# Kernel tuning notes

Measured on AMD Instinct MI355X. Metric: run time of the kernel, lower is better.

Reference implementation:

```python
import jax, jax.numpy as jnp
import numpy as np

NUM_NODES_FEAT = 400   # per-graph node count == input feature dim (fMRI ROIs)
F1 = 256
F2 = 256
NUM_GRAPHS = 256
N_TOTAL = NUM_GRAPHS * NUM_NODES_FEAT  # 102400 nodes
E_TOTAL = 4096000                      # ~40 avg degree


def setup_inputs() -> dict:
    key = jax.random.key(0)
    ks = jax.random.split(key, 8)
    x = jax.random.normal(ks[0], (N_TOTAL, NUM_NODES_FEAT), dtype=jnp.float32)
    edge_index = jax.random.randint(ks[1], (2, E_TOTAL), 0, N_TOTAL, dtype=jnp.int64)
    # PyG-style block-diagonal batch vector: 400 nodes per graph
    batch = jnp.repeat(jnp.arange(NUM_GRAPHS, dtype=jnp.int64), NUM_NODES_FEAT)
    # learned params (xavier-ish scale)
    def xavier(k, shape):
        fan_in, fan_out = shape[0], shape[1]
        s = jnp.sqrt(6.0 / (fan_in + fan_out))
        return jax.random.uniform(k, shape, jnp.float32, -s, s)
    W1 = xavier(ks[2], (NUM_NODES_FEAT, F1))
    b1 = jax.random.uniform(ks[3], (F1,), jnp.float32)
    W2 = xavier(ks[4], (F1, F2))
    b2 = jax.random.uniform(ks[5], (F2,), jnp.float32)
    Wm = xavier(ks[6], (2 * F2, 2))   # meanmax readout -> 2*f2 input
    bm = jax.random.uniform(ks[7], (2,), jnp.float32)
    return {"x": x, "edge_index": edge_index, "batch": batch,
            "num_graphs": NUM_GRAPHS,
            "W1": W1, "b1": b1, "W2": W2, "b2": b2, "Wm": Wm, "bm": bm}


def _gcn_conv(x, W, b, src, dst, deg_inv_sqrt, n):
    # PyG GCNConv: linear transform, then deg^{-1/2}-normalized scatter-add
    h = x @ W                                   # [N, f_out]
    norm = deg_inv_sqrt[src] * deg_inv_sqrt[dst]  # [E+N]
    msgs = h[src] * norm[:, None]               # gather + scale
    out = jax.ops.segment_sum(msgs, dst, num_segments=n)
    return out + b


def reference(x, edge_index, batch, num_graphs, W1, b1, W2, b2, Wm, bm):
    n = x.shape[0]
    loops = jnp.arange(n, dtype=edge_index.dtype)
    src = jnp.concatenate([edge_index[0], loops])  # add self-loops (PyG default)
    dst = jnp.concatenate([edge_index[1], loops])
    deg = jax.ops.segment_sum(jnp.ones_like(dst, dtype=x.dtype), dst, num_segments=n)
    deg_inv_sqrt = jnp.where(deg > 0, jax.lax.rsqrt(deg), 0.0)

    h = _gcn_conv(x, W1, b1, src, dst, deg_inv_sqrt, n)
    h = jax.nn.relu(h)
    # F.dropout(training=False) -> identity in eval mode
    h = _gcn_conv(h, W2, b2, src, dst, deg_inv_sqrt, n)

    # meanmax graph readout over batch segments
    g_sum = jax.ops.segment_sum(h, batch, num_segments=num_graphs)
    cnt = jax.ops.segment_sum(jnp.ones((n,), h.dtype), batch, num_segments=num_graphs)
    g_mean = g_sum / jnp.maximum(cnt, 1.0)[:, None]
    g_max = jax.ops.segment_max(h, batch, num_segments=num_graphs)
    g = jnp.concatenate([g_mean, g_max], axis=-1)  # [G, 2*f2]
    return g @ Wm + bm                             # [G, 2]
```

## Files before the change

### kernel.cpp

```cpp
#include <hip/hip_runtime.h>
#include <hip/hip_bf16.h>

#define N_NODES 102400
#define FEAT    400
#define F1      256
#define E_EDGES 4096000
#define NUM_G   256
#define NPG     400
#define NSLICE  8
#define NODES_PER_SLICE (NPG / NSLICE)

#define NBIN    400
#define BINCAP  12288
#define EPB     4096
#define BIN_BLOCKS (E_EDGES / EPB)
#define CVT1_BLOCKS 416
#define CVT2_BLOCKS 256
#define CVT_BLOCKS  (CVT1_BLOCKS + CVT2_BLOCKS)

typedef __attribute__((ext_vector_type(8))) short bfrag;
typedef __attribute__((ext_vector_type(4))) float ffrag;
typedef __attribute__((ext_vector_type(4))) short s4;

__device__ inline short f2b(float f) {
    __hip_bfloat16 h = __float2bfloat16(f);
    return *reinterpret_cast<short*>(&h);
}

#define ACC(uu) { auto vl = __builtin_amdgcn_cvt_pk_f32_fp8(uu, false); \
                  auto vh = __builtin_amdgcn_cvt_pk_f32_fp8(uu, true);  \
                  a0 += vl[0]; a1 += vl[1]; a2 += vh[0]; a3 += vh[1]; }

__global__ __launch_bounds__(256) void k_binA(const int* __restrict__ ei,
                                              int* __restrict__ binfill,
                                              int2* __restrict__ binbuf,
                                              const float* __restrict__ W1,
                                              const float* __restrict__ W2,
                                              short* __restrict__ Wt1,
                                              short* __restrict__ Wt2) {
    const int t = threadIdx.x;
    if (blockIdx.x < BIN_BLOCKS) {
        __shared__ int h[NBIN], base[NBIN], cur[NBIN];
        const int e0 = blockIdx.x * EPB;
        for (int b = t; b < NBIN; b += 256) h[b] = 0;
        __syncthreads();
#pragma unroll 4
        for (int k = 0; k < 16; ++k) {
            int d = ei[E_EDGES + e0 + k * 256 + t];
            atomicAdd(&h[d >> 8], 1);
        }
        __syncthreads();
        for (int b = t; b < NBIN; b += 256) {
            base[b] = atomicAdd(&binfill[b], h[b]);
            cur[b]  = 0;
        }
        __syncthreads();
#pragma unroll 4
        for (int k = 0; k < 16; ++k) {
            int e = e0 + k * 256 + t;
            int s = ei[e];
            int d = ei[E_EDGES + e];
            int bin = d >> 8;
            int idx = base[bin] + atomicAdd(&cur[bin], 1);
            if (idx < BINCAP) binbuf[(size_t)bin * BINCAP + idx] = make_int2(s, d);
        }
    } else {
        int cb = blockIdx.x - BIN_BLOCKS;
        if (cb < CVT1_BLOCKS) {
            int idx = cb * 256 + t;
            int n = idx / 416, k = idx - n * 416;
            float v = (k < 400) ? W1[(size_t)k * 256 + n] : 0.f;
            Wt1[idx] = f2b(v);
        } else {
            int idx = (cb - CVT1_BLOCKS) * 256 + t;
            int n = idx >> 8, k = idx & 255;
            Wt2[idx] = f2b(W2[(size_t)k * 256 + n]);
        }
    }
}

__global__ __launch_bounds__(512) void k_binscan(const int* __restrict__ binfill,
                                                 int* __restrict__ binbase) {
    __shared__ int s[512];
    int t = threadIdx.x;
    int v = (t < NBIN) ? binfill[t] : 0;
    s[t] = v;
    __syncthreads();
    for (int off = 1; off < 512; off <<= 1) {
        int u = (t >= off) ? s[t - off] : 0;
        __syncthreads();
        s[t] += u;
        __syncthreads();
    }
    if (t < NBIN) binbase[t] = s[t] - v;
}

__global__ __launch_bounds__(256) void k_bcnt(const int* __restrict__ binfill,
                                              const int* __restrict__ binbase,
                                              const int2* __restrict__ binbuf,
                                              int* __restrict__ row_start,
                                              float* __restrict__ dis) {
    __shared__ int h[256], sc[256];
    const int b = blockIdx.x, t = threadIdx.x;
    h[t] = 0;
    __syncthreads();
    int n = binfill[b]; if (n > BINCAP) n = BINCAP;
    const int2* p = binbuf + (size_t)b * BINCAP;
    for (int i = t; i < n; i += 256) atomicAdd(&h[p[i].y & 255], 1);
    __syncthreads();
    int deg = h[t];
    sc[t] = deg;
    __syncthreads();
    for (int off = 1; off < 256; off <<= 1) {
        int u = (t >= off) ? sc[t - off] : 0;
        __syncthreads();
        sc[t] += u;
        __syncthreads();
    }
    int node = b * 256 + t;
    row_start[node] = binbase[b] + sc[t] - deg;
    dis[node] = rsqrtf((float)(deg + 1));
    if (b == NBIN - 1 && t == 255) row_start[N_NODES] = binbase[b] + sc[t];
}

template<bool AF32>
__device__ void mm_body(int bm, int bn,
                        const void* __restrict__ Ap,
                        const short* __restrict__ Wt,
                        const float* __restrict__ dis,
                        int Kreal, int Kpad,
                        unsigned char* __restrict__ Cp) {
    __shared__ short As[128][40];
    __shared__ short Bs[128][40];
    const int t    = threadIdx.x;
    const int lane = t & 63;
    const int w    = t >> 6;
    const int wm   = w >> 1, wn = w & 1;
    const int m0   = bm * 128;
    const int n0   = bn * 128;
    const int sr   = t >> 1;
    const int sh   = (t & 1) * 16;

    ffrag acc[4][4];
#pragma unroll
    for (int i = 0; i < 4; ++i)
#pragma unroll
        for (int j = 0; j < 4; ++j) {
            ffrag z = {0.f, 0.f, 0.f, 0.f};
            acc[i][j] = z;
        }

    const int rl = lane & 15;
    const int kc = (lane >> 4) * 8;

    for (int k0 = 0; k0 < Kpad; k0 += 32) {
        short av[16], bv[16];
        if constexpr (AF32) {
            const float* A = (const float*)Ap;
            const float* arow = A + (size_t)(m0 + sr) * Kreal + k0 + sh;
#pragma unroll
            for (int c = 0; c < 4; ++c) {
                float4 v;
                if (k0 + sh + c * 4 < Kreal) v = *(const float4*)(arow + c * 4);
                else                         v = make_float4(0.f, 0.f, 0.f, 0.f);
                av[c * 4 + 0] = f2b(v.x);
                av[c * 4 + 1] = f2b(v.y);
                av[c * 4 + 2] = f2b(v.z);
                av[c * 4 + 3] = f2b(v.w);
            }
        } else {
            const short* A = (const short*)Ap;
            const short* arow = A + (size_t)(m0 + sr) * Kpad + k0 + sh;
            *(bfrag*)&av[0] = *(const bfrag*)arow;
            *(bfrag*)&av[8] = *(const bfrag*)(arow + 8);
        }
        const short* brow = Wt + (size_t)(n0 + sr) * Kpad + k0 + sh;
        *(bfrag*)&bv[0] = *(const bfrag*)brow;
        *(bfrag*)&bv[8] = *(const bfrag*)(brow + 8);

        __syncthreads();
        *(bfrag*)&As[sr][sh]     = *(bfrag*)&av[0];
        *(bfrag*)&As[sr][sh + 8] = *(bfrag*)&av[8];
        *(bfrag*)&Bs[sr][sh]     = *(bfrag*)&bv[0];
        *(bfrag*)&Bs[sr][sh + 8] = *(bfrag*)&bv[8];
        __syncthreads();

        bfrag a[4], b[4];
#pragma unroll
        for (int i = 0; i < 4; ++i) a[i] = *(const bfrag*)&As[wm * 64 + i * 16 + rl][kc];
#pragma unroll
        for (int j = 0; j < 4; ++j) b[j] = *(const bfrag*)&Bs[wn * 64 + j * 16 + rl][kc];
#pragma unroll
        for (int i = 0; i < 4; ++i)
#pragma unroll
            for (int j = 0; j < 4; ++j)
                acc[i][j] = __builtin_amdgcn_mfma_f32_16x16x32_bf16(a[i], b[j], acc[i][j], 0, 0, 0);
    }

    const int rh = lane >> 4;
    float scale[4][4];
#pragma unroll
    for (int i = 0; i < 4; ++i)
#pragma unroll
        for (int q = 0; q < 4; ++q)
            scale[i][q] = dis[m0 + wm * 64 + i * 16 + rh * 4 + q];

#pragma unroll
    for (int i = 0; i < 4; ++i)
#pragma unroll
        for (int j = 0; j < 4; ++j) {
            int col  = n0 + wn * 64 + j * 16 + rl;
            int rowb = m0 + wm * 64 + i * 16 + rh * 4;
#pragma unroll
            for (int q = 0; q < 4; ++q) {
                float v = acc[i][j][q] * scale[i][q];
                int p = __builtin_amdgcn_cvt_pk_fp8_f32(v, 0.f, 0, false);
                Cp[(size_t)(rowb + q) * 256 + col] = (unsigned char)(p & 0xff);
            }
        }
}

__global__ __launch_bounds__(256) void k_fillmm(const int* __restrict__ binfill,
                                                const int2* __restrict__ binbuf,
                                                const int* __restrict__ row_start,
                                                int* __restrict__ csr,
                                                const float* __restrict__ x,
                                                const short* __restrict__ Wt1,
                                                const float* __restrict__ dis,
                                                unsigned char* __restrict__ P8) {
    if (blockIdx.x < NBIN) {
        __shared__ int rs[256], cur[256];
        const int b = blockIdx.x, t = threadIdx.x;
        rs[t]  = row_start[b * 256 + t];
        cur[t] = 0;
        __syncthreads();
        int n = binfill[b]; if (n > BINCAP) n = BINCAP;
        const int2* p = binbuf + (size_t)b * BINCAP;
        for (int i = t; i < n; i += 256) {
            int2 e = p[i];
            int dl = e.y & 255;
            int pos = atomicAdd(&cur[dl], 1);
            csr[rs[dl] + pos] = e.x;
        }
    } else {
        int bx = blockIdx.x - NBIN;
        mm_body<true>(bx >> 1, bx & 1, (const void*)x, Wt1, dis, 400, 416, P8);
    }
}

__global__ __launch_bounds__(256) void k_mm2(const short* __restrict__ Pb,
                                             const short* __restrict__ Wt2,
                                             const float* __restrict__ dis,
                                             unsigned char* __restrict__ P8) {
    mm_body<false>(blockIdx.x, blockIdx.y, (const void*)Pb, Wt2, dis, 256, 256, P8);
}

__global__ __launch_bounds__(256) void k_agg8(const unsigned int* __restrict__ h8,
                                              const float* __restrict__ dis,
                                              const int* __restrict__ row_start,
                                              const int* __restrict__ csr,
                                              const float* __restrict__ bias,
                                              short* __restrict__ out) {
    const int w = threadIdx.x >> 6;
    const int t = threadIdx.x & 63;
    const int i = blockIdx.x * 4 + w;
    float di = dis[i];
    unsigned int u = h8[(size_t)i * 64 + t];
    auto lo = __builtin_amdgcn_cvt_pk_f32_fp8(u, false);
    auto hi = __builtin_amdgcn_cvt_pk_f32_fp8(u, true);
    float a0 = lo[0], a1 = lo[1], a2 = hi[0], a3 = hi[1];

    const int beg = row_start[i], end = row_start[i + 1];
    const int* row = csr + beg;
    const int n = end - beg;
    int j = 0;
    for (; j + 8 <= n; j += 8) {
        unsigned int uu[8];
#pragma unroll
        for (int k = 0; k < 8; ++k) uu[k] = h8[(size_t)row[j + k] * 64 + t];
#pragma unroll
        for (int k = 0; k < 8; ++k) ACC(uu[k])
    }
    for (; j + 4 <= n; j += 4) {
        unsigned int uu[4];
#pragma unroll
        for (int k = 0; k < 4; ++k) uu[k] = h8[(size_t)row[j + k] * 64 + t];
#pragma unroll
        for (int k = 0; k < 4; ++k) ACC(uu[k])
    }
    for (; j < n; ++j) {
        unsigned int uv = h8[(size_t)row[j] * 64 + t];
        ACC(uv)
    }
    float4 bb = *(const float4*)(bias + t * 4);
    s4 o;
    o[0] = f2b(fmaxf(fmaf(di, a0, bb.x), 0.f));
    o[1] = f2b(fmaxf(fmaf(di, a1, bb.y), 0.f));
    o[2] = f2b(fmaxf(fmaf(di, a2, bb.z), 0.f));
    o[3] = f2b(fmaxf(fmaf(di, a3, bb.w), 0.f));
    *(s4*)(out + (size_t)i * 256 + t * 4) = o;
}

__global__ __launch_bounds__(256) void k_agg2f(const unsigned int* __restrict__ h8,
                                               const float* __restrict__ dis,
                                               const int* __restrict__ row_start,
                                               const int* __restrict__ csr,
                                               const float* __restrict__ bias,
                                               float* __restrict__ partial) {
    const int g     = blockIdx.x;
    const int slice = blockIdx.y;
    const int t     = threadIdx.x;
    const int w     = t >> 6;
    const int lane  = t & 63;

    float4 bb = *(const float4*)(bias + lane * 4);
    float sm[4] = {0.f, 0.f, 0.f, 0.f};
    float mx[4] = {-3.402823466e38f, -3.402823466e38f, -3.402823466e38f, -3.402823466e38f};

    const int r0 = slice * NODES_PER_SLICE;
    for (int r = r0 + w; r < r0 + NODES_PER_SLICE; r += 4) {
        int i = g * NPG + r;
        float di = dis[i];
        unsigned int u = h8[(size_t)i * 64 + lane];
        auto lo = __builtin_amdgcn_cvt_pk_f32_fp8(u, false);
        auto hi = __builtin_amdgcn_cvt_pk_f32_fp8(u, true);
        float a0 = lo[0], a1 = lo[1], a2 = hi[0], a3 = hi[1];

        const int beg = row_start[i], end = row_start[i + 1];
        const int* row = csr + beg;
        const int n = end - beg;
        int j = 0;
        for (; j + 8 <= n; j += 8) {
            unsigned int uu[8];
#pragma unroll
            for (int k = 0; k < 8; ++k) uu[k] = h8[(size_t)row[j + k] * 64 + lane];
#pragma unroll
            for (int k = 0; k < 8; ++k) ACC(uu[k])
        }
        for (; j + 4 <= n; j += 4) {
            unsigned int uu[4];
#pragma unroll
            for (int k = 0; k < 4; ++k) uu[k] = h8[(size_t)row[j + k] * 64 + lane];
#pragma unroll
            for (int k = 0; k < 4; ++k) ACC(uu[k])
        }
        for (; j < n; ++j) {
            unsigned int uv = h8[(size_t)row[j] * 64 + lane];
            ACC(uv)
        }
        float h0 = fmaf(di, a0, bb.x);
        float h1 = fmaf(di, a1, bb.y);
        float h2 = fmaf(di, a2, bb.z);
        float h3 = fmaf(di, a3, bb.w);
        sm[0] += h0; sm[1] += h1; sm[2] += h2; sm[3] += h3;
        mx[0] = fmaxf(mx[0], h0); mx[1] = fmaxf(mx[1], h1);
        mx[2] = fmaxf(mx[2], h2); mx[3] = fmaxf(mx[3], h3);
    }

    __shared__ float ls[4][256];
    __shared__ float lm[4][256];
#pragma unroll
    for (int k = 0; k < 4; ++k) {
        ls[w][lane * 4 + k] = sm[k];
        lm[w][lane * 4 + k] = mx[k];
    }
    __syncthreads();
    if (w == 0) {
        float* base = partial + ((size_t)g * NSLICE + slice) * 512;
#pragma unroll
        for (int k = 0; k < 4; ++k) {
            int f = lane * 4 + k;
            base[f]       = ls[0][f] + ls[1][f] + ls[2][f] + ls[3][f];
            base[256 + f] = fmaxf(fmaxf(lm[0][f], lm[1][f]), fmaxf(lm[2][f], lm[3][f]));
        }
    }
}

__global__ __launch_bounds__(256) void k_final(const float* __restrict__ partial,
                                               const float* __restrict__ Wm,
                                               const float* __restrict__ bm,
                                               float* __restrict__ out) {
    int g = blockIdx.x, t = threadIdx.x;
    const float* pg = partial + (size_t)g * NSLICE * 512;
    float sum = 0.f, mxv = -3.402823466e38f;
#pragma unroll
    for (int s = 0; s < NSLICE; ++s) {
        sum += pg[s * 512 + t];
        mxv = fmaxf(mxv, pg[s * 512 + 256 + t]);
    }
    float mean = sum * (1.0f / NPG);
    float p0 = mean * Wm[t * 2 + 0] + mxv * Wm[(256 + t) * 2 + 0];
    float p1 = mean * Wm[t * 2 + 1] + mxv * Wm[(256 + t) * 2 + 1];
    __shared__ float2 red[256];
    red[t] = make_float2(p0, p1);
    __syncthreads();
    for (int s2 = 128; s2 > 0; s2 >>= 1) {
        if (t < s2) {
            red[t].x += red[t + s2].x;
            red[t].y += red[t + s2].y;
        }
        __syncthreads();
    }
    if (t == 0) {
        out[g * 2 + 0] = red[0].x + bm[0];
        out[g * 2 + 1] = red[0].y + bm[1];
    }
}

extern "C" void kernel_launch(void* const* d_in, const int* in_sizes, int n_in,
                              void* d_out, int out_size, void* d_ws, size_t ws_size,
                              hipStream_t stream) {
    const float* x  = (const float*)d_in[0];
    const int*   ei = (const int*)d_in[1];
    const float* W1 = (const float*)d_in[4];
    const float* b1 = (const float*)d_in[5];
    const float* W2 = (const float*)d_in[6];
    const float* b2 = (const float*)d_in[7];
    const float* Wm = (const float*)d_in[8];
    const float* bm = (const float*)d_in[9];
    float* out = (float*)d_out;

    char* ws = (char*)d_ws;
    size_t off = 0;
    auto alloc = [&](size_t bytes) {
        void* p = ws + off;
        off = (off + bytes + 255) & ~(size_t)255;
        return p;
    };
    int*   binfill   = (int*)alloc((size_t)NBIN * 4);
    int*   binbase   = (int*)alloc((size_t)NBIN * 4);
    int2*  binbuf    = (int2*)alloc((size_t)NBIN * BINCAP * 8);
    int*   row_start = (int*)alloc((size_t)(N_NODES + 1) * 4);
    float* dis       = (float*)alloc((size_t)N_NODES * 4);
    int*   csr       = (int*)alloc((size_t)E_EDGES * 4);
    short* Wt1       = (short*)alloc((size_t)256 * 416 * 2);
    short* Wt2       = (short*)alloc((size_t)256 * 256 * 2);
    unsigned char* P8 = (unsigned char*)alloc((size_t)N_NODES * F1);
    short* Pb        = (short*)alloc((size_t)N_NODES * F1 * 2);
    float* partialb  = (float*)alloc((size_t)NUM_G * NSLICE * 512 * 4);

    hipMemsetAsync(binfill, 0, (size_t)NBIN * 4, stream);
    k_binA<<<BIN_BLOCKS + CVT_BLOCKS, 256, 0, stream>>>(ei, binfill, binbuf,
                                                        W1, W2, Wt1, Wt2);
    k_binscan<<<1, 512, 0, stream>>>(binfill, binbase);
    k_bcnt<<<NBIN, 256, 0, stream>>>(binfill, binbase, binbuf, row_start, dis);
    k_fillmm<<<NBIN + 1600, 256, 0, stream>>>(binfill, binbuf, row_start, csr,
                                              x, Wt1, dis, P8);
    k_agg8<<<N_NODES / 4, 256, 0, stream>>>((const unsigned int*)P8, dis, row_start,
                                            csr, b1, Pb);
    k_mm2<<<dim3(800, 2), 256, 0, stream>>>(Pb, Wt2, dis, P8);
    k_agg2f<<<dim3(NUM_G, NSLICE), 256, 0, stream>>>((const unsigned int*)P8, dis,
                                                     row_start, csr, b2, partialb);
    k_final<<<NUM_G, 256, 0, stream>>>(partialb, Wm, bm, out);
}
```

Before: 548.6 us.

## Pack binned edges into 32-bit words, fold bin scan into count kernel, unroll gathers

Binned edges are stored as a single 32-bit word (24-bit source index plus 8-bit local destination) instead of an int2, halving binbuf write and read traffic in the binning, counting and CSR-fill kernels. The separate single-block prefix-scan kernel is removed; each k_bcnt block instead reduces the fill counts of all preceding bins to get its own base, saving a launch at the cost of redundant reads. The gather loops in both aggregation kernels are unrolled from 8 to 16 loads to keep more memory requests in flight, which raises register pressure. The packing assumes node indices fit in 24 bits, which holds for 102400 nodes.

New measurement: 552.0 us. About the same (+0.6%).

```diff
diff --git a/kernel.cpp b/kernel.cpp
--- a/kernel.cpp
+++ b/kernel.cpp
@@ -33,7 +33,7 @@
 
 __global__ __launch_bounds__(256) void k_binA(const int* __restrict__ ei,
                                               int* __restrict__ binfill,
-                                              int2* __restrict__ binbuf,
+                                              unsigned int* __restrict__ binbuf,
                                               const float* __restrict__ W1,
                                               const float* __restrict__ W2,
                                               short* __restrict__ Wt1,
@@ -58,11 +58,12 @@
 #pragma unroll 4
         for (int k = 0; k < 16; ++k) {
             int e = e0 + k * 256 + t;
-            int s = ei[e];
+            unsigned int s = (unsigned int)ei[e];
             int d = ei[E_EDGES + e];
             int bin = d >> 8;
             int idx = base[bin] + atomicAdd(&cur[bin], 1);
-            if (idx < BINCAP) binbuf[(size_t)bin * BINCAP + idx] = make_int2(s, d);
+            if (idx < BINCAP)
+                binbuf[(size_t)bin * BINCAP + idx] = s | ((unsigned int)(d & 255) << 24);
         }
     } else {
         int cb = blockIdx.x - BIN_BLOCKS;
@@ -79,34 +80,31 @@
     }
 }
 
-__global__ __launch_bounds__(512) void k_binscan(const int* __restrict__ binfill,
-                                                 int* __restrict__ binbase) {
-    __shared__ int s[512];
-    int t = threadIdx.x;
-    int v = (t < NBIN) ? binfill[t] : 0;
-    s[t] = v;
-    __syncthreads();
-    for (int off = 1; off < 512; off <<= 1) {
-        int u = (t >= off) ? s[t - off] : 0;
-        __syncthreads();
-        s[t] += u;
-        __syncthreads();
-    }
-    if (t < NBIN) binbase[t] = s[t] - v;
-}
-
 __global__ __launch_bounds__(256) void k_bcnt(const int* __restrict__ binfill,
-                                              const int* __restrict__ binbase,
-                                              const int2* __restrict__ binbuf,
+                                              const unsigned int* __restrict__ binbuf,
                                               int* __restrict__ row_start,
                                               float* __restrict__ dis) {
+    __shared__ int red[256];
     __shared__ int h[256], sc[256];
     const int b = blockIdx.x, t = threadIdx.x;
+
+    int v = 0;
+    if (t < b) v += binfill[t];
+    if (256 + t < b) v += binfill[256 + t];
+    red[t] = v;
+    __syncthreads();
+    for (int s = 128; s > 0; s >>= 1) {
+        if (t < s) red[t] += red[t + s];
+        __syncthreads();
+    }
+    const int binbase = red[0];
+    __syncthreads();
+
     h[t] = 0;
     __syncthreads();
     int n = binfill[b]; if (n > BINCAP) n = BINCAP;
-    const int2* p = binbuf + (size_t)b * BINCAP;
-    for (int i = t; i < n; i += 256) atomicAdd(&h[p[i].y & 255], 1);
+    const unsigned int* p = binbuf + (size_t)b * BINCAP;
+    for (int i = t; i < n; i += 256) atomicAdd(&h[p[i] >> 24], 1);
     __syncthreads();
     int deg = h[t];
     sc[t] = deg;
@@ -118,9 +116,9 @@
         __syncthreads();
     }
     int node = b * 256 + t;
-    row_start[node] = binbase[b] + sc[t] - deg;
+    row_start[node] = binbase + sc[t] - deg;
     dis[node] = rsqrtf((float)(deg + 1));
-    if (b == NBIN - 1 && t == 255) row_start[N_NODES] = binbase[b] + sc[t];
+    if (b == NBIN - 1 && t == 255) row_start[N_NODES] = binbase + sc[t];
 }
 
 template<bool AF32>
@@ -221,7 +219,7 @@
 }
 
 __global__ __launch_bounds__(256) void k_fillmm(const int* __restrict__ binfill,
-                                                const int2* __restrict__ binbuf,
+                                                const unsigned int* __restrict__ binbuf,
                                                 const int* __restrict__ row_start,
                                                 int* __restrict__ csr,
                                                 const float* __restrict__ x,
@@ -235,12 +233,12 @@
         cur[t] = 0;
         __syncthreads();
         int n = binfill[b]; if (n > BINCAP) n = BINCAP;
-        const int2* p = binbuf + (size_t)b * BINCAP;
+        const unsigned int* p = binbuf + (size_t)b * BINCAP;
         for (int i = t; i < n; i += 256) {
-            int2 e = p[i];
-            int dl = e.y & 255;
+            unsigned int e = p[i];
+            int dl = e >> 24;
             int pos = atomicAdd(&cur[dl], 1);
-            csr[rs[dl] + pos] = e.x;
+            csr[rs[dl] + pos] = (int)(e & 0x00FFFFFFu);
         }
     } else {
         int bx = blockIdx.x - NBIN;
@@ -274,12 +272,12 @@
     const int* row = csr + beg;
     const int n = end - beg;
     int j = 0;
-    for (; j + 8 <= n; j += 8) {
-        unsigned int uu[8];
-#pragma unroll
-        for (int k = 0; k < 8; ++k) uu[k] = h8[(size_t)row[j + k] * 64 + t];
-#pragma unroll
-        for (int k = 0; k < 8; ++k) ACC(uu[k])
+    for (; j + 16 <= n; j += 16) {
+        unsigned int uu[16];
+#pragma unroll
+        for (int k = 0; k < 16; ++k) uu[k] = h8[(size_t)row[j + k] * 64 + t];
+#pragma unroll
+        for (int k = 0; k < 16; ++k) ACC(uu[k])
     }
     for (; j + 4 <= n; j += 4) {
         unsigned int uu[4];
@@ -330,12 +328,12 @@
         const int* row = csr + beg;
         const int n = end - beg;
         int j = 0;
-        for (; j + 8 <= n; j += 8) {
-            unsigned int uu[8];
-#pragma unroll
-            for (int k = 0; k < 8; ++k) uu[k] = h8[(size_t)row[j + k] * 64 + lane];
-#pragma unroll
-            for (int k = 0; k < 8; ++k) ACC(uu[k])
+        for (; j + 16 <= n; j += 16) {
+            unsigned int uu[16];
+#pragma unroll
+            for (int k = 0; k < 16; ++k) uu[k] = h8[(size_t)row[j + k] * 64 + lane];
+#pragma unroll
+            for (int k = 0; k < 16; ++k) ACC(uu[k])
         }
         for (; j + 4 <= n; j += 4) {
             unsigned int uu[4];
@@ -427,23 +425,21 @@
         off = (off + bytes + 255) & ~(size_t)255;
         return p;
     };
-    int*   binfill   = (int*)alloc((size_t)NBIN * 4);
-    int*   binbase   = (int*)alloc((size_t)NBIN * 4);
-    int2*  binbuf    = (int2*)alloc((size_t)NBIN * BINCAP * 8);
-    int*   row_start = (int*)alloc((size_t)(N_NODES + 1) * 4);
-    float* dis       = (float*)alloc((size_t)N_NODES * 4);
-    int*   csr       = (int*)alloc((size_t)E_EDGES * 4);
-    short* Wt1       = (short*)alloc((size_t)256 * 416 * 2);
-    short* Wt2       = (short*)alloc((size_t)256 * 256 * 2);
-    unsigned char* P8 = (unsigned char*)alloc((size_t)N_NODES * F1);
-    short* Pb        = (short*)alloc((size_t)N_NODES * F1 * 2);
-    float* partialb  = (float*)alloc((size_t)NUM_G * NSLICE * 512 * 4);
+    int*          binfill   = (int*)alloc((size_t)NBIN * 4);
+    unsigned int* binbuf    = (unsigned int*)alloc((size_t)NBIN * BINCAP * 4);
+    int*          row_start = (int*)alloc((size_t)(N_NODES + 1) * 4);
+    float*        dis       = (float*)alloc((size_t)N_NODES * 4);
+    int*          csr       = (int*)alloc((size_t)E_EDGES * 4);
+    short*        Wt1       = (short*)alloc((size_t)256 * 416 * 2);
+    short*        Wt2       = (short*)alloc((size_t)256 * 256 * 2);
+    unsigned char* P8       = (unsigned char*)alloc((size_t)N_NODES * F1);
+    short*        Pb        = (short*)alloc((size_t)N_NODES * F1 * 2);
+    float*        partialb  = (float*)alloc((size_t)NUM_G * NSLICE * 512 * 4);
 
     hipMemsetAsync(binfill, 0, (size_t)NBIN * 4, stream);
     k_binA<<<BIN_BLOCKS + CVT_BLOCKS, 256, 0, stream>>>(ei, binfill, binbuf,
                                                         W1, W2, Wt1, Wt2);
-    k_binscan<<<1, 512, 0, stream>>>(binfill, binbase);
-    k_bcnt<<<NBIN, 256, 0, stream>>>(binfill, binbase, binbuf, row_start, dis);
+    k_bcnt<<<NBIN, 256, 0, stream>>>(binfill, binbuf, row_start, dis);
     k_fillmm<<<NBIN + 1600, 256, 0, stream>>>(binfill, binbuf, row_start, csr,
                                               x, Wt1, dis, P8);
     k_agg8<<<N_NODES / 4, 256, 0, stream>>>((const unsigned int*)P8, dis, row_start,
```
